# Kernel tuning notes

Measured on AMD Instinct MI355X. Metric: run time of the kernel, lower is better.

The kernel has to match this reference:

```python
import jax, jax.numpy as jnp
import numpy as np

EMB = 1024
HEADS = 16
HEAD_DIM = EMB // HEADS
HID = 4096
B, L = 1, 4096
EPS = 1e-5


def _layernorm(x, g, b):
    mu = jnp.mean(x, axis=-1, keepdims=True)
    var = jnp.mean(jnp.square(x - mu), axis=-1, keepdims=True)
    return (x - mu) * jax.lax.rsqrt(var + EPS) * g + b


def setup_inputs() -> dict:
    key = jax.random.key(0)
    ks = jax.random.split(key, 12)
    s = 0.02
    d = {
        "x": jax.random.normal(ks[0], (B, L, EMB), jnp.float32),
        "mask": jnp.ones((1, 1, L, L), jnp.int32),
        "Wq": jax.random.normal(ks[1], (EMB, EMB), jnp.float32) * s,
        "bq": jnp.zeros((EMB,), jnp.float32),
        "Wk": jax.random.normal(ks[2], (EMB, EMB), jnp.float32) * s,
        "bk": jnp.zeros((EMB,), jnp.float32),
        "Wv": jax.random.normal(ks[3], (EMB, EMB), jnp.float32) * s,
        "bv": jnp.zeros((EMB,), jnp.float32),
        "Wo": jax.random.normal(ks[4], (EMB, EMB), jnp.float32) * s,
        "bo": jnp.zeros((EMB,), jnp.float32),
        "g1": jnp.ones((EMB,), jnp.float32),
        "b1": jnp.zeros((EMB,), jnp.float32),
        "W1": jax.random.normal(ks[5], (EMB, HID), jnp.float32) * s,
        "bf1": jnp.zeros((HID,), jnp.float32),
        "W2": jax.random.normal(ks[6], (HID, EMB), jnp.float32) * s,
        "bf2": jnp.zeros((EMB,), jnp.float32),
        "g2": jnp.ones((EMB,), jnp.float32),
        "b2": jnp.zeros((EMB,), jnp.float32),
    }
    return d


def reference(x, mask, Wq, bq, Wk, bk, Wv, bv, Wo, bo, g1, b1, W1, bf1, W2, bf2, g2, b2):
    Bb, Ll, _ = x.shape
    # projections -> [B, H, L, Dh]
    def split(h):
        return h.reshape(Bb, Ll, HEADS, HEAD_DIM).transpose(0, 2, 1, 3)
    Q = split(x @ Wq + bq)
    K = split(x @ Wk + bk)
    V = split(x @ Wv + bv)
    scores = jnp.einsum("bhqd,bhkd->bhqk", Q, K) / jnp.sqrt(jnp.float32(HEAD_DIM))
    scores = jnp.where(mask == 0, jnp.float32(-1e9), scores)
    attn = jax.nn.softmax(scores, axis=-1)
    ctx = jnp.einsum("bhqk,bhkd->bhqd", attn, V)
    ctx = ctx.transpose(0, 2, 1, 3).reshape(Bb, Ll, EMB)
    attn_out = ctx @ Wo + bo
    x = _layernorm(x + attn_out, g1, b1)
    h = jax.nn.gelu(x @ W1 + bf1, approximate=False)
    ffn = h @ W2 + bf2
    x = _layernorm(x + ffn, g2, b2)
    return x
```

## Files before the change

### kernel.cpp

```cpp
#include <hip/hip_runtime.h>
#include <cstdint>
#include <cstddef>

#define EMB   1024
#define SEQ   4096
#define NHEAD 16
#define DHEAD 64
#define HIDD  4096
#define QSTR  2048

typedef float          f32x4 __attribute__((ext_vector_type(4)));
typedef short          s16x8 __attribute__((ext_vector_type(8)));
typedef unsigned short u16x4 __attribute__((ext_vector_type(4)));
typedef unsigned int   u32x2 __attribute__((ext_vector_type(2)));
typedef unsigned short u16;

__device__ __forceinline__ u16 f2bf(float f) {
  unsigned int u = __float_as_uint(f);
  u = u + 0x7FFFu + ((u >> 16) & 1u);
  return (u16)(u >> 16);
}

__device__ __forceinline__ float exp2_hw(float x) {
  return __builtin_amdgcn_exp2f(x);
}

__device__ __forceinline__ void gload16(const void* g, void* l) {
  __builtin_amdgcn_global_load_lds((const __attribute__((address_space(1))) void*)g,
                                   (__attribute__((address_space(3))) void*)l,
                                   16, 0, 0);
}

__global__ __launch_bounds__(256) void cvt_bf16_k(const float* __restrict__ in,
                                                  u16* __restrict__ out, int n4) {
  int idx = blockIdx.x * 256 + threadIdx.x;
  if (idx >= n4) return;
  f32x4 v = ((const f32x4*)in)[idx];
  u16x4 o;
#pragma unroll
  for (int r = 0; r < 4; ++r) o[r] = f2bf(v[r]);
  ((u16x4*)out)[idx] = o;
}

__global__ __launch_bounds__(256) void transpose_bf16_k(const float* __restrict__ in,
                                                        u16* __restrict__ out,
                                                        int K, int N) {
  __shared__ float tile[32][33];
  int n0 = blockIdx.x * 32, k0 = blockIdx.y * 32;
  for (int i = threadIdx.x; i < 1024; i += 256) {
    int r = i >> 5, c = i & 31;
    tile[r][c] = in[(size_t)(k0 + r) * N + n0 + c];
  }
  __syncthreads();
  for (int i = threadIdx.x; i < 1024; i += 256) {
    int r = i >> 5, c = i & 31;
    out[(size_t)(n0 + r) * K + k0 + c] = f2bf(tile[c][r]);
  }
}

__global__ __launch_bounds__(256) void transpose4_bf16_k(const float* __restrict__ W0,
                                                         const float* __restrict__ W1,
                                                         const float* __restrict__ W2,
                                                         const float* __restrict__ W3,
                                                         u16* __restrict__ outbase) {
  __shared__ float tile[32][33];
  int z = blockIdx.z;
  const float* in = (z == 0) ? W0 : (z == 1) ? W1 : (z == 2) ? W2 : W3;
  u16* out = outbase + (size_t)z * EMB * EMB;
  int n0 = blockIdx.x * 32, k0 = blockIdx.y * 32;
  for (int i = threadIdx.x; i < 1024; i += 256) {
    int r = i >> 5, c = i & 31;
    tile[r][c] = in[(size_t)(k0 + r) * EMB + n0 + c];
  }
  __syncthreads();
  for (int i = threadIdx.x; i < 1024; i += 256) {
    int r = i >> 5, c = i & 31;
    out[(size_t)(n0 + r) * EMB + k0 + c] = f2bf(tile[c][r]);
  }
}

template <int MODE, int BN>
__global__ __launch_bounds__(512, 4) void gemm_bt_k(const u16* __restrict__ A,
                                                    const u16* __restrict__ Bt,
                                                    const float* __restrict__ bias,
                                                    const float* __restrict__ res,
                                                    void* __restrict__ Out,
                                                    int M, int N, int K) {
  constexpr int AI  = (BN == 128) ? 4 : 2;
  constexpr int MST = (BN == 128) ? 64 : 32;
  __shared__ __align__(16) u16 As[2][128 * 32];
  __shared__ __align__(16) u16 Bs[2][BN * 32];
  int t = threadIdx.x, lane = t & 63, w = t >> 6;
  int wm = (BN == 128) ? (w >> 2) : (w >> 1);
  int wn = (BN == 128) ? (w & 3) : (w & 1);
  int m0 = blockIdx.y * 128, n0 = blockIdx.x * BN;
  int lr = lane & 15, lg = lane >> 4, lk = lg << 3;
  int srow = t >> 2;
  int scol = (t & 3) << 3;
  bool doB = (BN == 128) || (w < 4);

  const u16* gA = A  + (size_t)(m0 + srow) * K + scol;
  const u16* gB = Bt + (size_t)(n0 + (srow & (BN - 1))) * K + scol;

  f32x4 acc[AI][2];
#pragma unroll
  for (int i = 0; i < AI; ++i)
#pragma unroll
    for (int j = 0; j < 2; ++j)
#pragma unroll
      for (int r = 0; r < 4; ++r) acc[i][j][r] = 0.f;

  gload16(gA, (char*)As[0] + (w << 10));
  if (doB) gload16(gB, (char*)Bs[0] + (w << 10));

  int cur = 0;
  for (int k0 = 0; k0 < K; k0 += 32, cur ^= 1) {
    __syncthreads();
    if (k0 + 32 < K) {
      int kn = k0 + 32;
      gload16(gA + kn, (char*)As[cur ^ 1] + (w << 10));
      if (doB) gload16(gB + kn, (char*)Bs[cur ^ 1] + (w << 10));
    }

    s16x8 af[AI], bf[2];
#pragma unroll
    for (int i = 0; i < AI; ++i)
      af[i] = *(const s16x8*)&As[cur][(wm * MST + i * 16 + lr) * 32 + lk];
#pragma unroll
    for (int j = 0; j < 2; ++j)
      bf[j] = *(const s16x8*)&Bs[cur][(wn * 32 + j * 16 + lr) * 32 + lk];
#pragma unroll
    for (int i = 0; i < AI; ++i)
#pragma unroll
      for (int j = 0; j < 2; ++j)
        acc[i][j] = __builtin_amdgcn_mfma_f32_16x16x32_bf16(af[i], bf[j], acc[i][j], 0, 0, 0);
  }

  int orow0 = m0 + wm * MST, ocol0 = n0 + wn * 32;
#pragma unroll
  for (int i = 0; i < AI; ++i)
#pragma unroll
    for (int j = 0; j < 2; ++j) {
      int col = ocol0 + j * 16 + lr;
      float bcol;
      if (MODE == 3)      bcol = 0.f;
      else if (MODE == 4) bcol = (col < 1024) ? bias[col] : res[col - 1024];
      else                bcol = bias[col];
#pragma unroll
      for (int r = 0; r < 4; ++r) {
        int row = orow0 + i * 16 + lg * 4 + r;
        size_t idx = (size_t)row * N + col;
        if (MODE == 0) {
          ((u16*)Out)[idx] = f2bf(acc[i][j][r] + bcol);
        } else if (MODE == 1) {
          ((float*)Out)[idx] = acc[i][j][r] + bcol + res[idx];
        } else if (MODE == 2) {
          float v = acc[i][j][r] + bcol;
          float gl = 0.5f * v * (1.f + erff(v * 0.70710678118654752f));
          ((u16*)Out)[idx] = f2bf(gl);
        } else if (MODE == 3) {
          ((u16*)Out)[idx] = f2bf(acc[i][j][r] + bias[row]);
        } else {
          float v = acc[i][j][r] + bcol;
          ((u16*)Out)[idx] = f2bf(col < 1024 ? v * 0.18033688011112042f : v);
        }
      }
    }
}

__global__ __launch_bounds__(512) void attn_k(const u16* __restrict__ Qb,
                                              const u16* __restrict__ Kb,
                                              const u16* __restrict__ Vt,
                                              u16* __restrict__ ctx) {
  __shared__ __align__(16) u16 Ks[3][64 * 64];
  __shared__ __align__(16) u16 Vs[3][64 * 64];
  int t = threadIdx.x, lane = t & 63, w = t >> 6;
  int b = blockIdx.x;
  int xcd = b & 7, slot = b >> 3;
  int h = 2 * xcd + (slot >> 5);
  int q0 = (slot & 31) * 128 + w * 16;
  int lr = lane & 15, lg = lane >> 4, lk = lg << 3;
  int swl = (lr & 7) << 4;

  int ssb = ((lane & 7) << 4) ^ ((lane >> 3) << 4);
  int srw = w * 8 + (lane >> 3);
  const u16* gK0 = Kb + (size_t)srw * QSTR + h * DHEAD + (ssb >> 1);
  const u16* gV0 = Vt + (size_t)(h * DHEAD + srw) * SEQ + (ssb >> 1);
  int dstb = w << 10;

  s16x8 aq[2];
#pragma unroll
  for (int kf = 0; kf < 2; ++kf)
    aq[kf] = *(const s16x8*)&Qb[(size_t)(q0 + lr) * QSTR + h * DHEAD + kf * 32 + lk];

  f32x4 o[4];
#pragma unroll
  for (int dj = 0; dj < 4; ++dj)
#pragma unroll
    for (int r = 0; r < 4; ++r) o[dj][r] = 0.f;
  float m_run = -3.0e38f, l_run = 0.f;

  gload16(gK0, (char*)Ks[0] + dstb);
  gload16(gV0, (char*)Vs[0] + dstb);
  __syncthreads();

  f32x4 stA[4], stB[4];
  {
    const char* Kc = (const char*)Ks[0];
#pragma unroll
    for (int nj = 0; nj < 4; ++nj) {
#pragma unroll
      for (int r = 0; r < 4; ++r) stA[nj][r] = 0.f;
      int rowb = (nj * 16 + lr) * 128;
#pragma unroll
      for (int kf = 0; kf < 2; ++kf) {
        s16x8 bk = *(const s16x8*)(Kc + rowb + ((kf * 64 + lg * 16) ^ swl));
        stA[nj] = __builtin_amdgcn_mfma_f32_16x16x32_bf16(bk, aq[kf], stA[nj], 0, 0, 0);
      }
    }
  }
  gload16(gK0 + (size_t)64 * QSTR, (char*)Ks[1] + dstb);
  gload16(gV0 + 64,                (char*)Vs[1] + dstb);

  int bc = 0, b1 = 1, b2 = 2;

  auto step = [&](int tt, f32x4 (&st)[4], f32x4 (&stN)[4]) {
    __syncthreads();
    if (tt + 2 < 64) {
      size_t ko = (size_t)(tt + 2) * 64;
      gload16(gK0 + ko * QSTR, (char*)Ks[0] + b2 * 8192 + dstb);
      gload16(gV0 + ko,        (char*)Vs[0] + b2 * 8192 + dstb);
    }
    if (tt + 1 < 64) {
      const char* Kc = (const char*)Ks[0] + b1 * 8192;
#pragma unroll
      for (int nj = 0; nj < 4; ++nj) {
#pragma unroll
        for (int r = 0; r < 4; ++r) stN[nj][r] = 0.f;
        int rowb = (nj * 16 + lr) * 128;
#pragma unroll
        for (int kf = 0; kf < 2; ++kf) {
          s16x8 bk = *(const s16x8*)(Kc + rowb + ((kf * 64 + lg * 16) ^ swl));
          stN[nj] = __builtin_amdgcn_mfma_f32_16x16x32_bf16(bk, aq[kf], stN[nj], 0, 0, 0);
        }
      }
    }
    float mx = st[0][0];
#pragma unroll
    for (int nj = 0; nj < 4; ++nj)
#pragma unroll
      for (int r = 0; r < 4; ++r) mx = fmaxf(mx, st[nj][r]);
    mx = fmaxf(mx, __shfl_xor(mx, 16));
    mx = fmaxf(mx, __shfl_xor(mx, 32));
    if (!__all(mx - m_run <= 8.f)) {
      float mn = fmaxf(m_run, mx);
      float fac = exp2_hw(m_run - mn);
      m_run = mn;
      l_run *= fac;
      float fq[4];
#pragma unroll
      for (int r = 0; r < 4; ++r) fq[r] = __shfl(fac, lg * 4 + r);
#pragma unroll
      for (int dj = 0; dj < 4; ++dj)
#pragma unroll
        for (int r = 0; r < 4; ++r) o[dj][r] *= fq[r];
    }
    float rsum = 0.f;
#pragma unroll
    for (int nj = 0; nj < 4; ++nj)
#pragma unroll
      for (int r = 0; r < 4; ++r) {
        float p = exp2_hw(st[nj][r] - m_run);
        st[nj][r] = p;
        rsum += p;
      }
    rsum += __shfl_xor(rsum, 16);
    rsum += __shfl_xor(rsum, 32);
    l_run += rsum;

    u32x2 pk[4];
#pragma unroll
    for (int nj = 0; nj < 4; ++nj) {
      unsigned int lo, hi;
      asm("v_cvt_pk_bf16_f32 %0, %1, %2" : "=v"(lo) : "v"(st[nj][0]), "v"(st[nj][1]));
      asm("v_cvt_pk_bf16_f32 %0, %1, %2" : "=v"(hi) : "v"(st[nj][2]), "v"(st[nj][3]));
      pk[nj][0] = lo; pk[nj][1] = hi;
    }

    const char* Vc = (const char*)Vs[0] + bc * 8192;
#pragma unroll
    for (int dj = 0; dj < 4; ++dj) {
      int rowb = (dj * 16 + lr) * 128;
#pragma unroll
      for (int nj = 0; nj < 4; ++nj) {
        u32x2 vb = *(const u32x2*)(Vc + rowb + ((nj * 32 + lg * 8) ^ swl));
        asm volatile("s_nop 1\n\tv_mfma_f32_16x16x16_bf16 %0, %1, %2, %0"
                     : "+v"(o[dj]) : "v"(pk[nj]), "v"(vb));
      }
    }
    int tmp = bc; bc = b1; b1 = b2; b2 = tmp;
  };

  for (int tt = 0; tt < 64; tt += 2) {
    step(tt, stA, stB);
    step(tt + 1, stB, stA);
  }

  float linv = 1.f / l_run;
  float lq[4];
#pragma unroll
  for (int r = 0; r < 4; ++r) lq[r] = __shfl(linv, lg * 4 + r);
#pragma unroll
  for (int dj = 0; dj < 4; ++dj)
#pragma unroll
    for (int r = 0; r < 4; ++r)
      ctx[(size_t)(q0 + lg * 4 + r) * EMB + h * DHEAD + dj * 16 + lr] =
          f2bf(o[dj][r] * lq[r]);
}

__global__ __launch_bounds__(256) void ln_k(const float* __restrict__ hin,
                                            const float* __restrict__ g,
                                            const float* __restrict__ be,
                                            float* __restrict__ outf,
                                            u16* __restrict__ outb) {
  int row = blockIdx.x, t = threadIdx.x;
  int lane = t & 63, w = t >> 6;
  f32x4 v = ((const f32x4*)(hin + (size_t)row * EMB))[t];
  float s  = v[0] + v[1] + v[2] + v[3];
  float s2 = v[0] * v[0] + v[1] * v[1] + v[2] * v[2] + v[3] * v[3];
#pragma unroll
  for (int m = 1; m < 64; m <<= 1) { s += __shfl_xor(s, m); s2 += __shfl_xor(s2, m); }
  __shared__ float red[8];
  if (lane == 0) { red[w] = s; red[4 + w] = s2; }
  __syncthreads();
  s  = red[0] + red[1] + red[2] + red[3];
  s2 = red[4] + red[5] + red[6] + red[7];
  float mu  = s * (1.f / EMB);
  float var = s2 * (1.f / EMB) - mu * mu;
  float rs  = rsqrtf(var + 1e-5f);
  f32x4 gv = ((const f32x4*)g)[t];
  f32x4 bv = ((const f32x4*)be)[t];
  f32x4 y;
#pragma unroll
  for (int r = 0; r < 4; ++r) y[r] = (v[r] - mu) * rs * gv[r] + bv[r];
  if (outf) ((f32x4*)(outf + (size_t)row * EMB))[t] = y;
  if (outb) {
    u16x4 ob;
#pragma unroll
    for (int r = 0; r < 4; ++r) ob[r] = f2bf(y[r]);
    ((u16x4*)(outb + (size_t)row * EMB))[t] = ob;
  }
}

extern "C" void kernel_launch(void* const* d_in, const int* in_sizes, int n_in,
                              void* d_out, int out_size, void* d_ws, size_t ws_size,
                              hipStream_t stream) {
  const float* x  = (const float*)d_in[0];
  const float* Wq = (const float*)d_in[2];
  const float* bq = (const float*)d_in[3];
  const float* Wk = (const float*)d_in[4];
  const float* bk = (const float*)d_in[5];
  const float* Wv = (const float*)d_in[6];
  const float* bv = (const float*)d_in[7];
  const float* Wo = (const float*)d_in[8];
  const float* bo = (const float*)d_in[9];
  const float* g1 = (const float*)d_in[10];
  const float* b1 = (const float*)d_in[11];
  const float* W1 = (const float*)d_in[12];
  const float* bf1 = (const float*)d_in[13];
  const float* W2 = (const float*)d_in[14];
  const float* bf2 = (const float*)d_in[15];
  const float* g2 = (const float*)d_in[16];
  const float* b2 = (const float*)d_in[17];

  char* ws = (char*)d_ws;
  const size_t MB = (size_t)1 << 20;
  u16*   wqt = (u16*)(ws + 0 * MB);
  u16*   wvt = (u16*)(ws + 4 * MB);
  u16*   wot = (u16*)(ws + 6 * MB);
  u16*   w1t = (u16*)(ws + 8 * MB);
  u16*   w2t = (u16*)(ws + 16 * MB);
  u16*   xb  = (u16*)(ws + 24 * MB);
  u16*   QKb = (u16*)(ws + 32 * MB);
  u16*   VtG = (u16*)(ws + 48 * MB);
  u16*   ctx = (u16*)(ws + 56 * MB);
  float* h1  = (float*)(ws + 64 * MB);
  float* x1  = (float*)(ws + 80 * MB);
  u16*   x1b = (u16*)(ws + 96 * MB);
  u16*   hid = (u16*)(ws + 32 * MB);
  float* h2  = (float*)(ws + 64 * MB);

  cvt_bf16_k<<<dim3(SEQ * EMB / 4 / 256), 256, 0, stream>>>(x, xb, SEQ * EMB / 4);
  transpose4_bf16_k<<<dim3(EMB / 32, EMB / 32, 4), 256, 0, stream>>>(Wq, Wk, Wv, Wo, wqt);
  transpose_bf16_k<<<dim3(HIDD / 32, EMB / 32), 256, 0, stream>>>(W1, w1t, EMB, HIDD);
  transpose_bf16_k<<<dim3(EMB / 32, HIDD / 32), 256, 0, stream>>>(W2, w2t, HIDD, EMB);

  gemm_bt_k<4, 128><<<dim3(QSTR / 128, SEQ / 128), 512, 0, stream>>>(xb, wqt, bq, bk, QKb, SEQ, QSTR, EMB);
  gemm_bt_k<3, 64><<<dim3(SEQ / 64, EMB / 128), 512, 0, stream>>>(wvt, xb, bv, nullptr, VtG, EMB, SEQ, EMB);

  attn_k<<<dim3(512), 512, 0, stream>>>(QKb, QKb + 1024, VtG, ctx);

  gemm_bt_k<1, 64><<<dim3(EMB / 64, SEQ / 128), 512, 0, stream>>>(ctx, wot, bo, x, h1, SEQ, EMB, EMB);
  ln_k<<<dim3(SEQ), 256, 0, stream>>>(h1, g1, b1, x1, x1b);
  gemm_bt_k<2, 128><<<dim3(HIDD / 128, SEQ / 128), 512, 0, stream>>>(x1b, w1t, bf1, nullptr, hid, SEQ, HIDD, EMB);
  gemm_bt_k<1, 64><<<dim3(EMB / 64, SEQ / 128), 512, 0, stream>>>(hid, w2t, bf2, x1, h2, SEQ, EMB, HIDD);
  ln_k<<<dim3(SEQ), 256, 0, stream>>>(h2, g2, b2, (float*)d_out, nullptr);
}
```

Baseline: 336.3 us.

## Split attention KV range in two per block and merge partials in a second kernel

The attention kernel now launches twice as many blocks, each covering half of the key/value sequence, and writes unnormalized fp32 partial outputs plus running max and sum. A new merge kernel combines the two halves with log-sum-exp rescaling and writes the bf16 context. The goal is better occupancy and load balance across the GPU's compute units. The kernel also drops the triple-buffered, software-pipelined QK^T schedule for a simpler double-buffered loop with a sync per tile. In exchange it adds an extra launch, fp32 partial-result traffic, and possibly less latency hiding.

```diff
diff --git a/kernel.cpp b/kernel.cpp
--- a/kernel.cpp
+++ b/kernel.cpp
@@ -171,14 +171,18 @@
 __global__ __launch_bounds__(512) void attn_k(const u16* __restrict__ Qb,
                                               const u16* __restrict__ Kb,
                                               const u16* __restrict__ Vt,
-                                              u16* __restrict__ ctx) {
-  __shared__ __align__(16) u16 Ks[3][64 * 64];
-  __shared__ __align__(16) u16 Vs[3][64 * 64];
+                                              float* __restrict__ Op,
+                                              float* __restrict__ mlb) {
+  __shared__ __align__(16) u16 Ks[2][64 * 64];
+  __shared__ __align__(16) u16 Vs[2][64 * 64];
   int t = threadIdx.x, lane = t & 63, w = t >> 6;
   int b = blockIdx.x;
   int xcd = b & 7, slot = b >> 3;
-  int h = 2 * xcd + (slot >> 5);
-  int q0 = (slot & 31) * 128 + w * 16;
+  int h = 2 * xcd + (slot >> 6);
+  int rem = slot & 63;
+  int qb = rem >> 1, half = rem & 1;
+  int q0 = qb * 128 + w * 16;
+  int kv0 = half * (SEQ / 2);
   int lr = lane & 15, lg = lane >> 4, lk = lg << 3;
   int swl = (lr & 7) << 4;
 
@@ -200,51 +204,34 @@
     for (int r = 0; r < 4; ++r) o[dj][r] = 0.f;
   float m_run = -3.0e38f, l_run = 0.f;
 
-  gload16(gK0, (char*)Ks[0] + dstb);
-  gload16(gV0, (char*)Vs[0] + dstb);
+  gload16(gK0 + (size_t)kv0 * QSTR, (char*)Ks[0] + dstb);
+  gload16(gV0 + kv0,                (char*)Vs[0] + dstb);
   __syncthreads();
 
-  f32x4 stA[4], stB[4];
-  {
-    const char* Kc = (const char*)Ks[0];
+  int cur = 0;
+  int kend = kv0 + SEQ / 2;
+  for (int kb = kv0; kb < kend; kb += 64) {
+    if (kb + 64 < kend) {
+      size_t ko = (size_t)(kb + 64);
+      gload16(gK0 + ko * QSTR, (char*)Ks[cur ^ 1] + dstb);
+      gload16(gV0 + ko,        (char*)Vs[cur ^ 1] + dstb);
+    }
+    const char* Kc = (const char*)Ks[cur];
+    const char* Vc = (const char*)Vs[cur];
+
+    f32x4 st[4];
 #pragma unroll
     for (int nj = 0; nj < 4; ++nj) {
 #pragma unroll
-      for (int r = 0; r < 4; ++r) stA[nj][r] = 0.f;
+      for (int r = 0; r < 4; ++r) st[nj][r] = 0.f;
       int rowb = (nj * 16 + lr) * 128;
 #pragma unroll
       for (int kf = 0; kf < 2; ++kf) {
         s16x8 bk = *(const s16x8*)(Kc + rowb + ((kf * 64 + lg * 16) ^ swl));
-        stA[nj] = __builtin_amdgcn_mfma_f32_16x16x32_bf16(bk, aq[kf], stA[nj], 0, 0, 0);
+        st[nj] = __builtin_amdgcn_mfma_f32_16x16x32_bf16(bk, aq[kf], st[nj], 0, 0, 0);
       }
     }
-  }
-  gload16(gK0 + (size_t)64 * QSTR, (char*)Ks[1] + dstb);
-  gload16(gV0 + 64,                (char*)Vs[1] + dstb);
-
-  int bc = 0, b1 = 1, b2 = 2;
-
-  auto step = [&](int tt, f32x4 (&st)[4], f32x4 (&stN)[4]) {
-    __syncthreads();
-    if (tt + 2 < 64) {
-      size_t ko = (size_t)(tt + 2) * 64;
-      gload16(gK0 + ko * QSTR, (char*)Ks[0] + b2 * 8192 + dstb);
-      gload16(gV0 + ko,        (char*)Vs[0] + b2 * 8192 + dstb);
-    }
-    if (tt + 1 < 64) {
-      const char* Kc = (const char*)Ks[0] + b1 * 8192;
-#pragma unroll
-      for (int nj = 0; nj < 4; ++nj) {
-#pragma unroll
-        for (int r = 0; r < 4; ++r) stN[nj][r] = 0.f;
-        int rowb = (nj * 16 + lr) * 128;
-#pragma unroll
-        for (int kf = 0; kf < 2; ++kf) {
-          s16x8 bk = *(const s16x8*)(Kc + rowb + ((kf * 64 + lg * 16) ^ swl));
-          stN[nj] = __builtin_amdgcn_mfma_f32_16x16x32_bf16(bk, aq[kf], stN[nj], 0, 0, 0);
-        }
-      }
-    }
+
     float mx = st[0][0];
 #pragma unroll
     for (int nj = 0; nj < 4; ++nj)
@@ -287,7 +274,6 @@
       pk[nj][0] = lo; pk[nj][1] = hi;
     }
 
-    const char* Vc = (const char*)Vs[0] + bc * 8192;
 #pragma unroll
     for (int dj = 0; dj < 4; ++dj) {
       int rowb = (dj * 16 + lr) * 128;
@@ -298,24 +284,44 @@
                      : "+v"(o[dj]) : "v"(pk[nj]), "v"(vb));
       }
     }
-    int tmp = bc; bc = b1; b1 = b2; b2 = tmp;
-  };
-
-  for (int tt = 0; tt < 64; tt += 2) {
-    step(tt, stA, stB);
-    step(tt + 1, stB, stA);
-  }
-
-  float linv = 1.f / l_run;
-  float lq[4];
-#pragma unroll
-  for (int r = 0; r < 4; ++r) lq[r] = __shfl(linv, lg * 4 + r);
+
+    __syncthreads();
+    cur ^= 1;
+  }
+
 #pragma unroll
   for (int dj = 0; dj < 4; ++dj)
 #pragma unroll
     for (int r = 0; r < 4; ++r)
-      ctx[(size_t)(q0 + lg * 4 + r) * EMB + h * DHEAD + dj * 16 + lr] =
-          f2bf(o[dj][r] * lq[r]);
+      Op[((size_t)b * 128 + w * 16 + lg * 4 + r) * 64 + dj * 16 + lr] = o[dj][r];
+  if (lane < 16) {
+    mlb[((size_t)b * 128 + w * 16 + lr) * 2]     = m_run;
+    mlb[((size_t)b * 128 + w * 16 + lr) * 2 + 1] = l_run;
+  }
+}
+
+__global__ __launch_bounds__(256) void attn_merge_k(const float* __restrict__ Op,
+                                                    const float* __restrict__ mlb,
+                                                    u16* __restrict__ ctx) {
+  int t = threadIdx.x;
+  int idx = blockIdx.x * 16 + (t >> 4);
+  int h = idx >> 12, r = idx & 4095;
+  int qb = r >> 7, rl = r & 127;
+  int base = ((h & 1) << 6) + (qb << 1);
+  int b0 = (base + 0) * 8 + (h >> 1);
+  int b1 = (base + 1) * 8 + (h >> 1);
+  int d4 = (t & 15) << 2;
+  float m0 = mlb[((size_t)b0 * 128 + rl) * 2],     l0 = mlb[((size_t)b0 * 128 + rl) * 2 + 1];
+  float m1 = mlb[((size_t)b1 * 128 + rl) * 2],     l1 = mlb[((size_t)b1 * 128 + rl) * 2 + 1];
+  float m  = fmaxf(m0, m1);
+  float f0 = exp2_hw(m0 - m), f1 = exp2_hw(m1 - m);
+  float linv = 1.f / (l0 * f0 + l1 * f1);
+  f32x4 a = *(const f32x4*)(Op + ((size_t)b0 * 128 + rl) * 64 + d4);
+  f32x4 c = *(const f32x4*)(Op + ((size_t)b1 * 128 + rl) * 64 + d4);
+  u16x4 ob;
+#pragma unroll
+  for (int i = 0; i < 4; ++i) ob[i] = f2bf((a[i] * f0 + c[i] * f1) * linv);
+  *(u16x4*)(ctx + (size_t)r * EMB + h * DHEAD + d4) = ob;
 }
 
 __global__ __launch_bounds__(256) void ln_k(const float* __restrict__ hin,
@@ -389,6 +395,8 @@
   u16*   x1b = (u16*)(ws + 96 * MB);
   u16*   hid = (u16*)(ws + 32 * MB);
   float* h2  = (float*)(ws + 64 * MB);
+  float* Opart = (float*)(ws + 64 * MB);
+  float* mlbuf = (float*)(ws + 24 * MB);
 
   cvt_bf16_k<<<dim3(SEQ * EMB / 4 / 256), 256, 0, stream>>>(x, xb, SEQ * EMB / 4);
   transpose4_bf16_k<<<dim3(EMB / 32, EMB / 32, 4), 256, 0, stream>>>(Wq, Wk, Wv, Wo, wqt);
@@ -398,7 +406,8 @@
   gemm_bt_k<4, 128><<<dim3(QSTR / 128, SEQ / 128), 512, 0, stream>>>(xb, wqt, bq, bk, QKb, SEQ, QSTR, EMB);
   gemm_bt_k<3, 64><<<dim3(SEQ / 64, EMB / 128), 512, 0, stream>>>(wvt, xb, bv, nullptr, VtG, EMB, SEQ, EMB);
 
-  attn_k<<<dim3(512), 512, 0, stream>>>(QKb, QKb + 1024, VtG, ctx);
+  attn_k<<<dim3(1024), 512, 0, stream>>>(QKb, QKb + 1024, VtG, Opart, mlbuf);
+  attn_merge_k<<<dim3(SEQ * NHEAD / 16), 256, 0, stream>>>(Opart, mlbuf, ctx);
 
   gemm_bt_k<1, 64><<<dim3(EMB / 64, SEQ / 128), 512, 0, stream>>>(ctx, wot, bo, x, h1, SEQ, EMB, EMB);
   ln_k<<<dim3(SEQ), 256, 0, stream>>>(h1, g1, b1, x1, x1b);
```

Result: no change. 342.4 us (+1.8%).
